# Optimization experiments

Hardware: AMD Instinct MI355X
Metric: run time of the kernel (lower is better)

## Reference

```python
import jax, jax.numpy as jnp
import numpy as np

B, H, S, D = 2, 16, 2048, 64

def setup_inputs() -> dict:
    key = jax.random.key(0)
    kq, kk, kv = jax.random.split(key, 3)
    q = jax.random.normal(kq, (B, H, S, D), dtype=jnp.float32)
    k = jax.random.normal(kk, (B, H, S, D), dtype=jnp.float32)
    v = jax.random.normal(kv, (B, H, S, D), dtype=jnp.float32)
    mask = jnp.tril(jnp.ones((S, S), dtype=bool))  # causal, broadcast over B,H
    return {"q": q, "k": k, "v": v, "mask": mask}

def reference(q, k, v, mask):
    d_k = q.shape[-1]
    # [..., num_q, num_kv]
    qk = jnp.einsum('bhqd,bhkd->bhqk', q, k) / jnp.sqrt(jnp.asarray(d_k, q.dtype))
    qk = jnp.where(mask, qk, -jnp.inf)
    attn = jax.nn.softmax(qk, axis=-1)
    return jnp.einsum('bhqk,bhkd->bhqd', attn, v)
```

## Files before the change

### kernel.cpp

```cpp
#include <hip/hip_runtime.h>

#define SS 2048
#define DD 64
#define BH 32
#define QSCALE 0.1803368801f
#define BUFS 8448

typedef __attribute__((ext_vector_type(8))) short short8;
typedef __attribute__((ext_vector_type(4))) float floatx4;

__device__ __forceinline__ short f2bf(float x) {
  union { float f; unsigned u; } un; un.f = x;
  unsigned r = (un.u + 0x7FFFu + ((un.u >> 16) & 1u)) >> 16;
  return (short)r;
}
__device__ __forceinline__ short f2bf_fast(float x) {
  union { float f; unsigned u; } un; un.f = x;
  return (short)((un.u + 0x8000u) >> 16);
}
__device__ __forceinline__ float fexp2(float x) {
  return __builtin_amdgcn_exp2f(x);
}
__device__ __forceinline__ void gload16(const short* g, short* l) {
  __builtin_amdgcn_global_load_lds(
      (const __attribute__((address_space(1))) void*)g,
      (__attribute__((address_space(3))) void*)l, 16, 0, 0);
}
#define MFMA __builtin_amdgcn_mfma_f32_16x16x32_bf16

__device__ __forceinline__ int kperm(int c) {
  return (((c >> 2) & 1) << 4) + ((c >> 3) << 2) + (c & 3);
}

__global__ __launch_bounds__(256) void prep_kv(const float* __restrict__ K,
                                               const float* __restrict__ V,
                                               short* __restrict__ Kbf,
                                               short* __restrict__ Vtp) {
  __shared__ short Ts[64][72];
  const int bh = blockIdx.y;
  const int r0 = blockIdx.x * 64;
  const int t  = threadIdx.x;
  {
    const int r = t >> 2, c = (t & 3) * 16;
    const float* g = V + ((size_t)bh * SS + r0 + r) * DD + c;
    floatx4 a = *(const floatx4*)g;
    floatx4 b = *(const floatx4*)(g + 4);
    floatx4 cc = *(const floatx4*)(g + 8);
    floatx4 dd = *(const floatx4*)(g + 12);
    short8 x0, x1;
    x0[0]=f2bf(a[0]); x0[1]=f2bf(a[1]); x0[2]=f2bf(a[2]); x0[3]=f2bf(a[3]);
    x0[4]=f2bf(b[0]); x0[5]=f2bf(b[1]); x0[6]=f2bf(b[2]); x0[7]=f2bf(b[3]);
    x1[0]=f2bf(cc[0]);x1[1]=f2bf(cc[1]);x1[2]=f2bf(cc[2]);x1[3]=f2bf(cc[3]);
    x1[4]=f2bf(dd[0]);x1[5]=f2bf(dd[1]);x1[6]=f2bf(dd[2]);x1[7]=f2bf(dd[3]);
    *(short8*)&Ts[r][c] = x0;
    *(short8*)&Ts[r][c + 8] = x1;
  }
  {
    const size_t i = ((size_t)bh * SS + r0) * DD + (size_t)t * 16;
    floatx4 a = *(const floatx4*)(K + i);
    floatx4 b = *(const floatx4*)(K + i + 4);
    floatx4 cc = *(const floatx4*)(K + i + 8);
    floatx4 dd = *(const floatx4*)(K + i + 12);
    short8 x0, x1;
    x0[0]=f2bf(a[0]); x0[1]=f2bf(a[1]); x0[2]=f2bf(a[2]); x0[3]=f2bf(a[3]);
    x0[4]=f2bf(b[0]); x0[5]=f2bf(b[1]); x0[6]=f2bf(b[2]); x0[7]=f2bf(b[3]);
    x1[0]=f2bf(cc[0]);x1[1]=f2bf(cc[1]);x1[2]=f2bf(cc[2]);x1[3]=f2bf(cc[3]);
    x1[4]=f2bf(dd[0]);x1[5]=f2bf(dd[1]);x1[6]=f2bf(dd[2]);x1[7]=f2bf(dd[3]);
    *(short8*)(Kbf + i) = x0;
    *(short8*)(Kbf + i + 8) = x1;
  }
  __syncthreads();
  {
    const int d = t >> 2, cblk = (t & 3) * 16;
    short8 y0, y1;
    #pragma unroll
    for (int j = 0; j < 8; ++j) {
      const int c0 = cblk + j, c1 = cblk + 8 + j;
      y0[j] = Ts[(c0 & 32) + kperm(c0 & 31)][d];
      y1[j] = Ts[(c1 & 32) + kperm(c1 & 31)][d];
    }
    const int kt  = (r0 + cblk) >> 5;
    const int kin = cblk & 31;
    short* o = Vtp + (((size_t)bh * 64 + kt) * 64 + d) * 32 + kin;
    *(short8*)o = y0;
    *(short8*)(o + 8) = y1;
  }
}

__global__ __launch_bounds__(256, 4) void sdpa_fused(
    const float* __restrict__ Q, const short* __restrict__ Kbf,
    const short* __restrict__ Vtp, float* __restrict__ Og) {
  __shared__ __align__(16) short Sh[2][BUFS];

  const int tid  = threadIdx.x;
  const int w    = tid >> 6;
  const int lane = tid & 63;
  const int quad = lane >> 4;
  const int l16  = lane & 15;

  const int bh = blockIdx.x;
  const int y  = blockIdx.y;
  const int qt = (y < 8) ? (15 - y) : (y - 8);
  const int ktn = 4 * qt + 4;
  const int ktd = 4 * qt + w;
  const int qA  = qt * 128 + w * 32;
  const int qB  = qA + 16;

  const size_t base = (size_t)bh * SS * DD;
  const short* kbase = Kbf + base;
  const short* vtb   = Vtp + base;

  {
    const short* gk = kbase + w * 512 + lane * 8;
    gload16(gk,        &Sh[0][w * 544]);
    gload16(gk + 2048, &Sh[0][2176 + w * 544]);
    const short* gv = vtb + w * 512 + lane * 8;
    gload16(gv,        &Sh[0][4352 + w * 512]);
    gload16(gv + 2048, &Sh[0][6400 + w * 512]);
  }

  short8 qaA0, qaA1, qaB0, qaB1;
  {
    const float* ga = Q + base + (size_t)(qA + l16) * DD + quad * 8;
    const float* gb = Q + base + (size_t)(qB + l16) * DD + quad * 8;
    floatx4 a0 = *(const floatx4*)ga,        a1 = *(const floatx4*)(ga + 4);
    floatx4 a2 = *(const floatx4*)(ga + 32), a3 = *(const floatx4*)(ga + 36);
    floatx4 b0 = *(const floatx4*)gb,        b1 = *(const floatx4*)(gb + 4);
    floatx4 b2 = *(const floatx4*)(gb + 32), b3 = *(const floatx4*)(gb + 36);
    #pragma unroll
    for (int j = 0; j < 4; ++j) {
      qaA0[j] = f2bf(a0[j] * QSCALE); qaA0[4 + j] = f2bf(a1[j] * QSCALE);
      qaA1[j] = f2bf(a2[j] * QSCALE); qaA1[4 + j] = f2bf(a3[j] * QSCALE);
      qaB0[j] = f2bf(b0[j] * QSCALE); qaB0[4 + j] = f2bf(b1[j] * QSCALE);
      qaB1[j] = f2bf(b2[j] * QSCALE); qaB1[4 + j] = f2bf(b3[j] * QSCALE);
    }
  }

  short8 ones;
  #pragma unroll
  for (int j = 0; j < 8; ++j) ones[j] = (short)0x3F80;

  floatx4 z = {0.f, 0.f, 0.f, 0.f};
  floatx4 oA0 = z, oA1 = z, oA2 = z, oA3 = z;
  floatx4 oB0 = z, oB1 = z, oB2 = z, oB3 = z;
  floatx4 sA = z, sB = z;

  int nb = 0;
  for (int ktp = 0; ktp < ktn; ktp += 2) {
    __asm__ volatile("s_waitcnt vmcnt(0)" ::: "memory");
    __syncthreads();

    if (ktp + 2 < ktn) {
      const short* gk = kbase + (size_t)(ktp + 2) * 2048 + w * 512 + lane * 8;
      gload16(gk,        &Sh[nb ^ 1][w * 544]);
      gload16(gk + 2048, &Sh[nb ^ 1][2176 + w * 544]);
      const short* gv = vtb + (size_t)(ktp + 2) * 2048 + w * 512 + lane * 8;
      gload16(gv,        &Sh[nb ^ 1][4352 + w * 512]);
      gload16(gv + 2048, &Sh[nb ^ 1][6400 + w * 512]);
    }

    #pragma unroll
    for (int j = 0; j < 2; ++j) {
      const int kt = ktp + j;
      if (kt <= ktd) {
        const short* lb = &Sh[nb][j * 2176];
        const short* vb = &Sh[nb][4352 + j * 2048];
        const int kro = (l16 >> 3) * 544 + (l16 & 7) * 64 + quad * 8;
        short8 kb00 = *(const short8*)(lb + kro);
        short8 kb01 = *(const short8*)(lb + kro + 32);
        short8 kb10 = *(const short8*)(lb + kro + 1088);
        short8 kb11 = *(const short8*)(lb + kro + 1120);
        const int vro = l16 * 32 + quad * 8;
        short8 vt0 = *(const short8*)(vb + vro);
        short8 vt1 = *(const short8*)(vb + vro + 512);
        short8 vt2 = *(const short8*)(vb + vro + 1024);
        short8 vt3 = *(const short8*)(vb + vro + 1536);

        floatx4 tA0 = z, tA1 = z, tB0 = z, tB1 = z;
        tA0 = MFMA(kb00, qaA0, tA0, 0, 0, 0); tA0 = MFMA(kb01, qaA1, tA0, 0, 0, 0);
        tA1 = MFMA(kb10, qaA0, tA1, 0, 0, 0); tA1 = MFMA(kb11, qaA1, tA1, 0, 0, 0);
        tB0 = MFMA(kb00, qaB0, tB0, 0, 0, 0); tB0 = MFMA(kb01, qaB1, tB0, 0, 0, 0);
        tB1 = MFMA(kb10, qaB0, tB1, 0, 0, 0); tB1 = MFMA(kb11, qaB1, tB1, 0, 0, 0);

        if (kt == ktd) {
          const int kq = quad * 4;
          #pragma unroll
          for (int r = 0; r < 4; ++r) {
            tA0[r] = (kq + r      <= l16)      ? tA0[r] : -1e30f;
            tA1[r] = (kq + r + 16 <= l16)      ? tA1[r] : -1e30f;
            tB0[r] = (kq + r      <= l16 + 16) ? tB0[r] : -1e30f;
            tB1[r] = (kq + r      <= l16)      ? tB1[r] : -1e30f;
          }
        }

        short8 paA, paB;
        #pragma unroll
        for (int r = 0; r < 4; ++r) {
          paA[r]     = f2bf_fast(fexp2(tA0[r]));
          paA[4 + r] = f2bf_fast(fexp2(tA1[r]));
          paB[r]     = f2bf_fast(fexp2(tB0[r]));
          paB[4 + r] = f2bf_fast(fexp2(tB1[r]));
        }

        sA = MFMA(ones, paA, sA, 0, 0, 0);
        sB = MFMA(ones, paB, sB, 0, 0, 0);

        oA0 = MFMA(vt0, paA, oA0, 0, 0, 0); oA1 = MFMA(vt1, paA, oA1, 0, 0, 0);
        oA2 = MFMA(vt2, paA, oA2, 0, 0, 0); oA3 = MFMA(vt3, paA, oA3, 0, 0, 0);
        oB0 = MFMA(vt0, paB, oB0, 0, 0, 0); oB1 = MFMA(vt1, paB, oB1, 0, 0, 0);
        oB2 = MFMA(vt2, paB, oB2, 0, 0, 0); oB3 = MFMA(vt3, paB, oB3, 0, 0, 0);
      }
    }
    nb ^= 1;
  }

  const float invA = 1.0f / sA[0];
  const float invB = 1.0f / sB[0];
  oA0 *= invA; oA1 *= invA; oA2 *= invA; oA3 *= invA;
  oB0 *= invB; oB1 *= invB; oB2 *= invB; oB3 *= invB;

  float* ra = Og + base + (size_t)(qA + l16) * DD + quad * 4;
  float* rb = Og + base + (size_t)(qB + l16) * DD + quad * 4;
  *(floatx4*)(ra)      = oA0;
  *(floatx4*)(ra + 16) = oA1;
  *(floatx4*)(ra + 32) = oA2;
  *(floatx4*)(ra + 48) = oA3;
  *(floatx4*)(rb)      = oB0;
  *(floatx4*)(rb + 16) = oB1;
  *(floatx4*)(rb + 32) = oB2;
  *(floatx4*)(rb + 48) = oB3;
}

extern "C" void kernel_launch(void* const* d_in, const int* in_sizes, int n_in,
                              void* d_out, int out_size, void* d_ws, size_t ws_size,
                              hipStream_t stream) {
  (void)in_sizes; (void)n_in; (void)out_size; (void)ws_size;
  const float* q = (const float*)d_in[0];
  const float* k = (const float*)d_in[1];
  const float* v = (const float*)d_in[2];
  float* o = (float*)d_out;

  short* Kbf = (short*)d_ws;
  short* Vtp = Kbf + (size_t)BH * SS * DD;

  prep_kv<<<dim3(SS / 64, BH), 256, 0, stream>>>(k, v, Kbf, Vtp);
  sdpa_fused<<<dim3(BH, 16), 256, 0, stream>>>(q, Kbf, Vtp, o);
}
```

Baseline: 131.6 us.

## Triple-buffer K/V LDS tiles with partial vmcnt waits and raised wave priority

Switches the K/V shared-memory staging from double to triple buffering. Loads are issued two stages ahead and each stage waits only for the older group (vmcnt(4)) instead of draining all outstanding loads. The __syncthreads is replaced by a raw s_barrier, and wave priority is raised around the MFMA compute section. Shared memory per block grows by half, which may limit how many blocks fit per CU under the 4-block launch bound. The raw barrier and partial waits rely on the exact count of outstanding loads per stage.

```diff
diff --git a/kernel.cpp b/kernel.cpp
--- a/kernel.cpp
+++ b/kernel.cpp
@@ -90,7 +90,7 @@
 __global__ __launch_bounds__(256, 4) void sdpa_fused(
     const float* __restrict__ Q, const short* __restrict__ Kbf,
     const short* __restrict__ Vtp, float* __restrict__ Og) {
-  __shared__ __align__(16) short Sh[2][BUFS];
+  __shared__ __align__(16) short Sh[3][BUFS];
 
   const int tid  = threadIdx.x;
   const int w    = tid >> 6;
@@ -102,6 +102,7 @@
   const int y  = blockIdx.y;
   const int qt = (y < 8) ? (15 - y) : (y - 8);
   const int ktn = 4 * qt + 4;
+  const int np  = ktn >> 1;
   const int ktd = 4 * qt + w;
   const int qA  = qt * 128 + w * 32;
   const int qB  = qA + 16;
@@ -136,6 +137,15 @@
     }
   }
 
+  {
+    const short* gk = kbase + (size_t)2 * 2048 + w * 512 + lane * 8;
+    gload16(gk,        &Sh[1][w * 544]);
+    gload16(gk + 2048, &Sh[1][2176 + w * 544]);
+    const short* gv = vtb + (size_t)2 * 2048 + w * 512 + lane * 8;
+    gload16(gv,        &Sh[1][4352 + w * 512]);
+    gload16(gv + 2048, &Sh[1][6400 + w * 512]);
+  }
+
   short8 ones;
   #pragma unroll
   for (int j = 0; j < 8; ++j) ones[j] = (short)0x3F80;
@@ -145,26 +155,29 @@
   floatx4 oB0 = z, oB1 = z, oB2 = z, oB3 = z;
   floatx4 sA = z, sB = z;
 
-  int nb = 0;
-  for (int ktp = 0; ktp < ktn; ktp += 2) {
-    __asm__ volatile("s_waitcnt vmcnt(0)" ::: "memory");
-    __syncthreads();
-
-    if (ktp + 2 < ktn) {
-      const short* gk = kbase + (size_t)(ktp + 2) * 2048 + w * 512 + lane * 8;
-      gload16(gk,        &Sh[nb ^ 1][w * 544]);
-      gload16(gk + 2048, &Sh[nb ^ 1][2176 + w * 544]);
-      const short* gv = vtb + (size_t)(ktp + 2) * 2048 + w * 512 + lane * 8;
-      gload16(gv,        &Sh[nb ^ 1][4352 + w * 512]);
-      gload16(gv + 2048, &Sh[nb ^ 1][6400 + w * 512]);
-    }
-
+  int cur = 0;
+  for (int p = 0; p < np; ++p) {
+    if (p + 1 < np) { __asm__ volatile("s_waitcnt vmcnt(4)" ::: "memory"); }
+    else            { __asm__ volatile("s_waitcnt vmcnt(0)" ::: "memory"); }
+    __asm__ volatile("s_barrier" ::: "memory");
+
+    if (p + 2 < np) {
+      int ib = cur + 2; if (ib >= 3) ib -= 3;
+      const short* gk = kbase + (size_t)(2 * p + 4) * 2048 + w * 512 + lane * 8;
+      gload16(gk,        &Sh[ib][w * 544]);
+      gload16(gk + 2048, &Sh[ib][2176 + w * 544]);
+      const short* gv = vtb + (size_t)(2 * p + 4) * 2048 + w * 512 + lane * 8;
+      gload16(gv,        &Sh[ib][4352 + w * 512]);
+      gload16(gv + 2048, &Sh[ib][6400 + w * 512]);
+    }
+
+    __builtin_amdgcn_s_setprio(1);
     #pragma unroll
     for (int j = 0; j < 2; ++j) {
-      const int kt = ktp + j;
+      const int kt = 2 * p + j;
       if (kt <= ktd) {
-        const short* lb = &Sh[nb][j * 2176];
-        const short* vb = &Sh[nb][4352 + j * 2048];
+        const short* lb = &Sh[cur][j * 2176];
+        const short* vb = &Sh[cur][4352 + j * 2048];
         const int kro = (l16 >> 3) * 544 + (l16 & 7) * 64 + quad * 8;
         short8 kb00 = *(const short8*)(lb + kro);
         short8 kb01 = *(const short8*)(lb + kro + 32);
@@ -211,7 +224,9 @@
         oB2 = MFMA(vt2, paB, oB2, 0, 0, 0); oB3 = MFMA(vt3, paB, oB3, 0, 0, 0);
       }
     }
-    nb ^= 1;
+    __builtin_amdgcn_s_setprio(0);
+
+    cur = (cur == 2) ? 0 : (cur + 1);
   }
 
   const float invA = 1.0f / sA[0];
```

New measurement: 138.2 us. 1.05x slower.
